# Performance work log

Hardware: AMD Instinct MI355X
Metric: run time of the kernel (lower is better)

## Reference

```python
import jax, jax.numpy as jnp
import numpy as np

V, E, U, D, B, T = 32000, 256, 512, 512, 32, 64


def setup_inputs() -> dict:
    key = jax.random.key(0)
    ks = jax.random.split(key, 12)
    g = lambda k, shape: (jax.random.normal(k, shape, jnp.float32) * 0.05)
    return dict(
        x=jax.random.randint(ks[0], (B, T), 0, V),
        emb=g(ks[1], (V, E)),
        Wxf=g(ks[2], (E, 4 * U)), Whf=g(ks[3], (U, 4 * U)), bf=jnp.zeros((4 * U,), jnp.float32),
        Wxb=g(ks[4], (E, 4 * U)), Whb=g(ks[5], (U, 4 * U)), bb=jnp.zeros((4 * U,), jnp.float32),
        W1=g(ks[6], (2 * U + D, 10)), b1=jnp.zeros((10,), jnp.float32),
        W2=g(ks[7], (10, 1)), b2=jnp.zeros((1,), jnp.float32),
        Wxd=g(ks[8], (2 * U, 4 * D)), Whd=g(ks[9], (D, 4 * D)), bd=jnp.zeros((4 * D,), jnp.float32),
        Wo=g(ks[10], (D, V)), bo=jnp.zeros((V,), jnp.float32),
    )


def lstm_cell(x_t, h, c, Wx, Wh, b):
    # Keras gate order: i, f, g(cell), o
    z = x_t @ Wx + h @ Wh + b
    i, f, g, o = jnp.split(z, 4, axis=-1)
    c = jax.nn.sigmoid(f) * c + jax.nn.sigmoid(i) * jnp.tanh(g)
    h = jax.nn.sigmoid(o) * jnp.tanh(c)
    return h, c


def lstm_seq(xs, Wx, Wh, b):
    # xs: [T, B, F] -> hidden states [T, B, units]
    units = Wh.shape[0]
    h0 = jnp.zeros((xs.shape[1], units), xs.dtype)

    def step(carry, x_t):
        h, c = lstm_cell(x_t, carry[0], carry[1], Wx, Wh, b)
        return (h, c), h

    _, hs = jax.lax.scan(step, (h0, h0), xs)
    return hs


def reference(x, emb, Wxf, Whf, bf, Wxb, Whb, bb, W1, b1, W2, b2, Wxd, Whd, bd, Wo, bo):
    Bsz, Tlen = x.shape
    xe = emb[x]                              # [B, T, E]
    xs = jnp.swapaxes(xe, 0, 1)              # [T, B, E]
    hf = lstm_seq(xs, Wxf, Whf, bf)          # forward direction
    hb = lstm_seq(xs[::-1], Wxb, Whb, bb)[::-1]  # backward direction
    a = jnp.swapaxes(jnp.concatenate([hf, hb], axis=-1), 0, 1)  # [B, T, 2U]
    du = Whd.shape[0]

    def dec_step(carry, _):
        h, c = carry
        s_rep = jnp.broadcast_to(h[:, None, :], (Bsz, Tlen, du))
        cat = jnp.concatenate([a, s_rep], axis=-1)              # [B, T, 2U+D]
        e = jax.nn.relu(jnp.tanh(cat @ W1 + b1) @ W2 + b2)      # [B, T, 1]
        score = jax.nn.softmax(e, axis=1)
        ctx = jnp.sum(score * a, axis=1)                        # [B, 2U]
        h, c = lstm_cell(ctx, h, c, Wxd, Whd, bd)
        out = jax.nn.softmax(h @ Wo + bo, axis=-1)              # [B, V]
        return (h, c), out

    init = (jnp.zeros((Bsz, du), a.dtype), jnp.zeros((Bsz, du), a.dtype))
    _, outs = jax.lax.scan(dec_step, init, None, length=Tlen)
    return jnp.swapaxes(outs, 0, 1)  # [B, T, V]
```

## Files before the change

kernel.cpp:

```cpp
#include <hip/hip_runtime.h>
#include <hip/hip_bf16.h>
#include <cstdint>

typedef float f32x4 __attribute__((ext_vector_type(4)));
typedef __bf16 bf16x8 __attribute__((ext_vector_type(8)));

__device__ __forceinline__ uint32_t bf1(float x) {
  uint32_t u = __float_as_uint(x);
  return (u + 0x7fffu + ((u >> 16) & 1u)) >> 16;
}
__device__ __forceinline__ uint32_t bpack(float lo, float hi) {
  return bf1(lo) | (bf1(hi) << 16);
}
__device__ __forceinline__ float blo(uint32_t u) { return __uint_as_float(u << 16); }
__device__ __forceinline__ float bhi(uint32_t u) { return __uint_as_float(u & 0xffff0000u); }
__device__ __forceinline__ float sigm(float x) {
  return __fdividef(1.f, 1.f + exp2f(x * -1.4426950408889634f));
}
__device__ __forceinline__ float tanhf_fast(float x) {
  float e2 = exp2f(x * 2.8853900817779268f);
  return 1.f - __fdividef(2.f, e2 + 1.f);
}

__device__ __forceinline__ float dot2bf(uint32_t a, uint32_t b, float acc) {
  asm("v_dot2_f32_bf16 %0, %1, %2, %0" : "+v"(acc) : "v"(a), "v"(b));
  return acc;
}

#define GLOAD_LDS16(g, l)                                                     \
  __builtin_amdgcn_global_load_lds(                                           \
      (const __attribute__((address_space(1))) void*)(g),                     \
      (__attribute__((address_space(3))) void*)(l), 16, 0, 0)

__global__ __launch_bounds__(256) void k0_enc(
    const float* __restrict__ Whf, const float* __restrict__ Whb,
    uint32_t* __restrict__ Wp)
{
  int p = blockIdx.x * 256 + threadIdx.x;
  int e = p & 3, c = (p >> 2) & 7, k4p = (p >> 5) & 63;
  int blk = (p >> 11) & 255, dir = p >> 19;
  int k2 = 4 * k4p + e;
  const float* W = dir ? Whb : Whf;
  int col = (c >> 1) * 512 + blk * 2 + (c & 1);
  float v0 = W[(size_t)(2 * k2) * 2048 + col];
  float v1 = W[(size_t)(2 * k2 + 1) * 2048 + col];
  Wp[p] = bpack(v0, v1);
}

__global__ __launch_bounds__(256) void k0_dec(
    const float* __restrict__ Whd, uint32_t* __restrict__ Wp)
{
  int p = blockIdx.x * 256 + threadIdx.x;
  int e = p & 3, cc = (p >> 2) & 31, q4 = (p >> 7) & 63, ug = p >> 13;
  int k2 = 4 * q4 + e;
  int col = (cc >> 3) * 512 + ug * 8 + (cc & 7);
  int k = 2 * k2;
  float v0 = Whd[(size_t)k * 2048 + col];
  float v1 = Whd[(size_t)(k + 1) * 2048 + col];
  Wp[p] = bpack(v0, v1);
}

__global__ __launch_bounds__(256) void k0_w1(
    const float* __restrict__ W1, uint32_t* __restrict__ W1pbAll)
{
  int p = blockIdx.x * 256 + threadIdx.x;
  int q = p / 12, j = p % 12;
  float v0 = (j < 10) ? W1[(size_t)(2 * q) * 10 + j] : 0.f;
  float v1 = (j < 10) ? W1[(size_t)(2 * q + 1) * 10 + j] : 0.f;
  W1pbAll[p] = bpack(v0, v1);
}

__global__ __launch_bounds__(256) void k1_embed_gemm(
    const int* __restrict__ x, const float* __restrict__ emb,
    const float* __restrict__ Wxf, const float* __restrict__ Wxb,
    const float* __restrict__ bfv, const float* __restrict__ bbv,
    float* __restrict__ Xf, float* __restrict__ Xb)
{
  __shared__ float As[32 * 260];
  __shared__ float Bs[32 * 128];
  __shared__ int xid[32];
  const int t = threadIdx.x;
  const int ty = blockIdx.y;
  const int c0 = blockIdx.x * 128;
  if (t < 32) xid[t] = x[t * 64 + ty];
  __syncthreads();
  for (int i = 0; i < 8; ++i) {
    int f4 = t + 256 * i;
    int r = f4 >> 6, k4 = (f4 & 63) << 2;
    float4 v = *(const float4*)(emb + (size_t)xid[r] * 256 + k4);
    *(float4*)(&As[r * 260 + k4]) = v;
  }
  const int isB = (c0 >= 2048);
  const float* Wsrc = isB ? Wxb : Wxf;
  const float* bias = isB ? bbv : bfv;
  const int cbase = c0 & 2047;
  float acc[4][4] = {};
  const int rq = t >> 5;
  const int cq = t & 31;
  for (int kc = 0; kc < 8; ++kc) {
    int k0 = kc * 32;
    __syncthreads();
    for (int i = 0; i < 4; ++i) {
      int f4 = t + 256 * i;
      int k = f4 >> 5, c4 = (f4 & 31) << 2;
      *(float4*)(&Bs[k * 128 + c4]) =
          *(const float4*)(Wsrc + (size_t)(k0 + k) * 2048 + cbase + c4);
    }
    __syncthreads();
#pragma unroll
    for (int kk = 0; kk < 32; ++kk) {
      float a0 = As[(4 * rq + 0) * 260 + k0 + kk];
      float a1 = As[(4 * rq + 1) * 260 + k0 + kk];
      float a2 = As[(4 * rq + 2) * 260 + k0 + kk];
      float a3 = As[(4 * rq + 3) * 260 + k0 + kk];
      float4 b = *(const float4*)(&Bs[kk * 128 + 4 * cq]);
      acc[0][0] += a0 * b.x; acc[0][1] += a0 * b.y; acc[0][2] += a0 * b.z; acc[0][3] += a0 * b.w;
      acc[1][0] += a1 * b.x; acc[1][1] += a1 * b.y; acc[1][2] += a1 * b.z; acc[1][3] += a1 * b.w;
      acc[2][0] += a2 * b.x; acc[2][1] += a2 * b.y; acc[2][2] += a2 * b.z; acc[2][3] += a2 * b.w;
      acc[3][0] += a3 * b.x; acc[3][1] += a3 * b.y; acc[3][2] += a3 * b.z; acc[3][3] += a3 * b.w;
    }
  }
  float* Xout = isB ? Xb : Xf;
  for (int i = 0; i < 4; ++i) {
    int c = cbase + 4 * cq + i;
    float bi = bias[c];
    for (int j = 0; j < 4; ++j) {
      int b_ = 4 * rq + j;
      Xout[((size_t)ty * 2048 + c) * 32 + b_] = acc[j][i] + bi;
    }
  }
}

__global__ __launch_bounds__(256) void k2_enc_step(
    const float* __restrict__ Xf, const float* __restrict__ Xb,
    const uint32_t* __restrict__ Wencp,
    const uint32_t* __restrict__ hfi, uint32_t* __restrict__ hfo,
    const uint32_t* __restrict__ hbi, uint32_t* __restrict__ hbo,
    float* __restrict__ cf, float* __restrict__ cb,
    ushort* __restrict__ aB, int step)
{
  __shared__ uint32_t hTp[256 * 32];
  __shared__ uint32_t Wsp[2048];
  __shared__ float zx[8 * 33];
  __shared__ float zbuf[32 * 9];
  __shared__ float hl[2 * 32];
  const int t = threadIdx.x;
  const int dir = blockIdx.x >> 8;
  const int blk = blockIdx.x & 255;
  const int u0 = blk * 2;
  const float* XF = dir ? Xb : Xf;
  const uint32_t* hin = dir ? hbi : hfi;
  uint32_t* hout = dir ? hbo : hfo;
  float* cst = dir ? cb : cf;
  const int ta = dir ? (63 - step) : step;
  const uint32_t* wsrc = Wencp + ((size_t)dir * 256 + blk) * 2048;

  for (int i = 0; i < 8; ++i) {
    int b4 = (t >> 6) * 64 + 256 * i;
    GLOAD_LDS16(hin + (size_t)(t + 256 * i) * 4, hTp + (size_t)b4 * 4);
  }
  for (int i = 0; i < 2; ++i) {
    int b4 = (t >> 6) * 64 + 256 * i;
    GLOAD_LDS16(wsrc + (size_t)(t + 256 * i) * 4, Wsp + (size_t)b4 * 4);
  }
  {
    int c = t >> 5, r = t & 31;
    int col = (c >> 1) * 512 + u0 + (c & 1);
    zx[c * 33 + r] = XF[((size_t)ta * 2048 + col) * 32 + r];
  }
  __syncthreads();
  const int r = t & 31, cc = t >> 5;
  float acc = zx[cc * 33 + r];
  const uint4* hT4 = (const uint4*)hTp;
  const uint4* Ws4 = (const uint4*)Wsp;
#pragma unroll 8
  for (int k4p = 0; k4p < 64; ++k4p) {
    uint4 ua = hT4[k4p * 32 + r];
    uint4 w = Ws4[k4p * 8 + cc];
    acc = dot2bf(ua.x, w.x, acc);
    acc = dot2bf(ua.y, w.y, acc);
    acc = dot2bf(ua.z, w.z, acc);
    acc = dot2bf(ua.w, w.w, acc);
  }
  zbuf[r * 9 + cc] = acc;
  __syncthreads();
  if (t < 64) {
    int rr = t & 31, j = t >> 5;
    float zi = zbuf[rr * 9 + j];
    float zf = zbuf[rr * 9 + 2 + j];
    float zg = zbuf[rr * 9 + 4 + j];
    float zo = zbuf[rr * 9 + 6 + j];
    int u = u0 + j;
    float cold = cst[u * 32 + rr];
    float cn = sigm(zf) * cold + sigm(zi) * tanhf_fast(zg);
    float h = sigm(zo) * tanhf_fast(cn);
    cst[u * 32 + rr] = cn;
    aB[((size_t)rr * 64 + ta) * 1024 + dir * 512 + u] = (ushort)bf1(h);
    hl[j * 32 + rr] = h;
  }
  __syncthreads();
  if (t < 32) {
    hout[(blk >> 2) * 128 + t * 4 + (blk & 3)] = bpack(hl[t], hl[32 + t]);
  }
}

__global__ __launch_bounds__(256) void k5_aw1(
    const ushort* __restrict__ aB, const uint32_t* __restrict__ W1pbAll,
    const float* __restrict__ b1, float* __restrict__ aw1)
{
  __shared__ uint32_t ar[512];
  __shared__ float ps[16 * 17];
  const int t = threadIdx.x;
  const uint32_t* aBu = (const uint32_t*)aB;
  for (int m = blockIdx.x; m < 2048; m += gridDim.x) {
    __syncthreads();
    *(uint2*)(&ar[t * 2]) = *(const uint2*)(aBu + (size_t)m * 512 + t * 2);
    __syncthreads();
    int j = t & 15, part = t >> 4;
    int jj = j < 10 ? j : 0;
    float s = 0.f;
#pragma unroll 8
    for (int q = part * 32; q < part * 32 + 32; ++q)
      s = dot2bf(ar[q], W1pbAll[q * 12 + jj], s);
    ps[part * 17 + j] = s;
    __syncthreads();
    if (t < 16) {
      float sum = 0.f;
      if (t < 10) {
        for (int p = 0; p < 16; ++p) sum += ps[p * 17 + t];
        sum += b1[t];
      }
      aw1[m * 16 + t] = sum;
    }
  }
}

__global__ __launch_bounds__(256) void k_wxdT(
    const float* __restrict__ Wxd, ushort* __restrict__ WxdT)
{
  __shared__ float tile[64 * 65];
  const int t = threadIdx.x;
  const int n0 = blockIdx.x * 64, k0 = blockIdx.y * 64;
  for (int i = 0; i < 16; ++i) {
    int p = t + 256 * i;
    int kk = p >> 6, nn = p & 63;
    tile[kk * 65 + nn] = Wxd[(size_t)(k0 + kk) * 2048 + n0 + nn];
  }
  __syncthreads();
  for (int i = 0; i < 4; ++i) {
    int p = t + 256 * i;
    int nn = p >> 4, k4 = (p & 15) * 4;
    ushort4 o;
    o.x = (ushort)bf1(tile[(k4 + 0) * 65 + nn]);
    o.y = (ushort)bf1(tile[(k4 + 1) * 65 + nn]);
    o.z = (ushort)bf1(tile[(k4 + 2) * 65 + nn]);
    o.w = (ushort)bf1(tile[(k4 + 3) * 65 + nn]);
    *(ushort4*)(WxdT + (size_t)(n0 + nn) * 1024 + k0 + k4) = o;
  }
}

__global__ __launch_bounds__(256) void kA_aprime(
    const ushort* __restrict__ WxdT, const ushort* __restrict__ aB,
    uint32_t* __restrict__ ApTb)
{
  __shared__ ushort As[128 * 64];
  __shared__ ushort Bs[128 * 64];
  const int t = threadIdx.x;
  const int lane = t & 63, w = t >> 6;
  const int wr = w >> 1, wc = w & 1;
  const int m0 = blockIdx.y * 128, n0 = blockIdx.x * 128;
  const int lrow = lane >> 3, s = lane & 7;
  const int quad = lane >> 4, l15 = lane & 15;
  f32x4 acc[4][4] = {};
  for (int kc = 0; kc < 16; ++kc) {
    const int k0 = kc * 64;
    __syncthreads();
    for (int i = 0; i < 4; ++i) {
      int row = w * 32 + i * 8 + lrow;
      int k8 = s ^ (row & 7);
      GLOAD_LDS16(WxdT + (size_t)(m0 + row) * 1024 + k0 + k8 * 8,
                  As + (w * 32 + i * 8) * 64);
      GLOAD_LDS16(aB + (size_t)(n0 + row) * 1024 + k0 + k8 * 8,
                  Bs + (w * 32 + i * 8) * 64);
    }
    __syncthreads();
#pragma unroll
    for (int ks = 0; ks < 2; ++ks) {
      bf16x8 af[4], bfr[4];
      int kq = ks * 4 + quad;
#pragma unroll
      for (int mi = 0; mi < 4; ++mi) {
        int row = wr * 64 + mi * 16 + l15;
        int slot = kq ^ (row & 7);
        af[mi] = *(const bf16x8*)(As + row * 64 + slot * 8);
      }
#pragma unroll
      for (int ni = 0; ni < 4; ++ni) {
        int row = wc * 64 + ni * 16 + l15;
        int slot = kq ^ (row & 7);
        bfr[ni] = *(const bf16x8*)(Bs + row * 64 + slot * 8);
      }
#pragma unroll
      for (int mi = 0; mi < 4; ++mi)
#pragma unroll
        for (int ni = 0; ni < 4; ++ni)
          acc[mi][ni] = __builtin_amdgcn_mfma_f32_16x16x32_bf16(
              af[mi], bfr[ni], acc[mi][ni], 0, 0, 0);
    }
  }
#pragma unroll
  for (int mi = 0; mi < 4; ++mi) {
    int mbase = m0 + wr * 64 + mi * 16 + quad * 4;
#pragma unroll
    for (int reg = 0; reg < 4; ++reg) {
      int m = mbase + reg;
#pragma unroll
      for (int ni = 0; ni < 4; ++ni) {
        int n = n0 + wc * 64 + ni * 16 + l15;
        float v = acc[mi][ni][reg];
        float v2 = __shfl_xor(v, 1);
        if (!(l15 & 1))
          ApTb[(size_t)m * 1024 + (n >> 1)] = bpack(v, v2);
      }
    }
  }
}

__global__ __launch_bounds__(256) void k4_dec_step(
    const uint32_t* __restrict__ ApTb, const float* __restrict__ aw1,
    const uint32_t* __restrict__ W1pb, const float* __restrict__ W2,
    const float* __restrict__ b2, const uint32_t* __restrict__ hdp_in,
    const uint32_t* __restrict__ Wdp, const float* __restrict__ bd,
    uint32_t* __restrict__ hdp_out, float* __restrict__ cd,
    ushort* __restrict__ HsB, int step)
{
  __shared__ uint32_t W1s[256 * 12];
  __shared__ uint32_t hdT[4096];
  __shared__ uint32_t Wsp[8192];
  __shared__ float ph[32 * 8 * 12];
  __shared__ float hw1[8 * 12];
  __shared__ float esc[8 * 65];
  __shared__ uint32_t escp[8 * 33];
  __shared__ float pm[8 * 9];
  __shared__ float mrow[8], srow[8];
  __shared__ float w2s[12];
  __shared__ float zbuf[8 * 33];
  __shared__ float hl[64];
  const int t = threadIdx.x;
  const int ug = blockIdx.x >> 2;
  const int rg = blockIdx.x & 3;
  const int u0 = ug * 8, r0 = rg * 8;
  for (int i = 0; i < 3; ++i) {
    int b4 = (t >> 6) * 64 + 256 * i;
    GLOAD_LDS16(W1pb + (size_t)(t + 256 * i) * 4, W1s + (size_t)b4 * 4);
  }
  for (int i = 0; i < 4; ++i) {
    int idx4 = t + 256 * i;
    int q4 = idx4 >> 3, rl = idx4 & 7;
    int b4 = (t >> 6) * 64 + 256 * i;
    GLOAD_LDS16(hdp_in + (size_t)(q4 * 32 + r0 + rl) * 4, hdT + (size_t)b4 * 4);
  }
  {
    const uint32_t* wsrc = Wdp + (size_t)ug * 8192;
    for (int i = 0; i < 8; ++i) {
      int b4 = (t >> 6) * 64 + 256 * i;
      GLOAD_LDS16(wsrc + (size_t)(t + 256 * i) * 4, Wsp + (size_t)b4 * 4);
    }
  }
  if (t < 12) w2s[t] = (t < 10) ? W2[t] : 0.f;
  __syncthreads();
  {
    const int rl = t & 7, kp = t >> 3;
    const uint4* hd4 = (const uint4*)hdT;
    float acc[10] = {};
    for (int q4 = kp * 2; q4 < kp * 2 + 2; ++q4) {
      uint4 u4 = hd4[q4 * 8 + rl];
      const uint32_t* w0 = &W1s[(4 * q4) * 12];
      const uint32_t* w1 = &W1s[(4 * q4 + 1) * 12];
      const uint32_t* w2p = &W1s[(4 * q4 + 2) * 12];
      const uint32_t* w3 = &W1s[(4 * q4 + 3) * 12];
#pragma unroll
      for (int j = 0; j < 10; ++j) {
        acc[j] = dot2bf(u4.x, w0[j], acc[j]);
        acc[j] = dot2bf(u4.y, w1[j], acc[j]);
        acc[j] = dot2bf(u4.z, w2p[j], acc[j]);
        acc[j] = dot2bf(u4.w, w3[j], acc[j]);
      }
    }
#pragma unroll
    for (int j = 0; j < 10; ++j) ph[(kp * 8 + rl) * 12 + j] = acc[j];
  }
  __syncthreads();
  if (t < 96) {
    int rl = t / 12, j = t % 12;
    float s = 0.f;
#pragma unroll
    for (int p = 0; p < 32; ++p) s += ph[(p * 8 + rl) * 12 + j];
    hw1[rl * 12 + j] = s;
  }
  __syncthreads();
  const float b2v = b2[0];
  for (int p = 0; p < 2; ++p) {
    int idx = t + 256 * p;
    int rl = idx >> 6, tt = idx & 63;
    size_t m = (size_t)(r0 + rl) * 64 + tt;
    const float4* aw = (const float4*)(aw1 + m * 16);
    float4 q0 = aw[0], q1 = aw[1], q2 = aw[2];
    const float* hw = &hw1[rl * 12];
    float e = b2v;
    e += tanhf_fast(q0.x + hw[0]) * w2s[0];
    e += tanhf_fast(q0.y + hw[1]) * w2s[1];
    e += tanhf_fast(q0.z + hw[2]) * w2s[2];
    e += tanhf_fast(q0.w + hw[3]) * w2s[3];
    e += tanhf_fast(q1.x + hw[4]) * w2s[4];
    e += tanhf_fast(q1.y + hw[5]) * w2s[5];
    e += tanhf_fast(q1.z + hw[6]) * w2s[6];
    e += tanhf_fast(q1.w + hw[7]) * w2s[7];
    e += tanhf_fast(q2.x + hw[8]) * w2s[8];
    e += tanhf_fast(q2.y + hw[9]) * w2s[9];
    esc[rl * 65 + tt] = fmaxf(e, 0.f);
  }
  __syncthreads();
  if (t < 64) {
    int rl = t >> 3, part = t & 7;
    float m = -1e30f;
    for (int i = 0; i < 8; ++i) m = fmaxf(m, esc[rl * 65 + part * 8 + i]);
    pm[rl * 9 + part] = m;
  }
  __syncthreads();
  if (t < 8) {
    float m = pm[t * 9];
    for (int p = 1; p < 8; ++p) m = fmaxf(m, pm[t * 9 + p]);
    mrow[t] = m;
  }
  __syncthreads();
  if (t < 64) {
    int rl = t >> 3, part = t & 7;
    float m = mrow[rl];
    float s = 0.f;
    for (int i = 0; i < 8; ++i) s += __expf(esc[rl * 65 + part * 8 + i] - m);
    pm[rl * 9 + part] = s;
  }
  __syncthreads();
  if (t < 8) {
    float s = 0.f;
    for (int p = 0; p < 8; ++p) s += pm[t * 9 + p];
    srow[t] = __fdividef(1.f, s);
  }
  __syncthreads();
  {
    int rl = t >> 5, q = t & 31;
    float m = mrow[rl], s = srow[rl];
    float v0 = __expf(esc[rl * 65 + 2 * q] - m) * s;
    float v1 = __expf(esc[rl * 65 + 2 * q + 1] - m) * s;
    escp[rl * 33 + q] = bpack(v0, v1);
  }
  __syncthreads();
  const int ccB = t >> 3, rl = t & 7;
  const int colg = (ccB >> 3) * 512 + u0 + (ccB & 7);
  float acc = 0.f;
  {
    const uint4* hd4 = (const uint4*)hdT;
    const uint4* wd4 = (const uint4*)Wsp;
#pragma unroll 8
    for (int q4 = 0; q4 < 64; ++q4) {
      uint4 ua = hd4[q4 * 8 + rl];
      uint4 ub = wd4[q4 * 32 + ccB];
      acc = dot2bf(ua.x, ub.x, acc);
      acc = dot2bf(ua.y, ub.y, acc);
      acc = dot2bf(ua.z, ub.z, acc);
      acc = dot2bf(ua.w, ub.w, acc);
    }
  }
  {
    const uint32_t* ap = ApTb + (size_t)colg * 1024 + (r0 + rl) * 32;
    const uint32_t* ep = &escp[rl * 33];
#pragma unroll
    for (int i8 = 0; i8 < 8; ++i8) {
      uint4 v = *(const uint4*)(ap + i8 * 4);
      acc = dot2bf(v.x, ep[4 * i8 + 0], acc);
      acc = dot2bf(v.y, ep[4 * i8 + 1], acc);
      acc = dot2bf(v.z, ep[4 * i8 + 2], acc);
      acc = dot2bf(v.w, ep[4 * i8 + 3], acc);
    }
  }
  zbuf[rl * 33 + ccB] = acc + bd[colg];
  __syncthreads();
  if (t < 64) {
    int j = t >> 3, rr = t & 7;
    int u = u0 + j, rgl = r0 + rr;
    float zi = zbuf[rr * 33 + j];
    float zf = zbuf[rr * 33 + 8 + j];
    float zg = zbuf[rr * 33 + 16 + j];
    float zo = zbuf[rr * 33 + 24 + j];
    float cold = cd[u * 32 + rgl];
    float cn = sigm(zf) * cold + sigm(zi) * tanhf_fast(zg);
    float h = sigm(zo) * tanhf_fast(cn);
    cd[u * 32 + rgl] = cn;
    HsB[(size_t)(step * 32 + rgl) * 512 + u] = (ushort)bf1(h);
    hl[j * 8 + rr] = h;
  }
  __syncthreads();
  if (t < 32) {
    int p = t >> 3, rr = t & 7;
    hdp_out[ug * 128 + (r0 + rr) * 4 + p] =
        bpack(hl[(2 * p) * 8 + rr], hl[(2 * p + 1) * 8 + rr]);
  }
}

__global__ __launch_bounds__(256) void k_woT(
    const float* __restrict__ Wo, ushort* __restrict__ WoT)
{
  __shared__ float tile[64 * 65];
  const int t = threadIdx.x;
  const int n0 = blockIdx.x * 64, k0 = blockIdx.y * 64;
  for (int i = 0; i < 16; ++i) {
    int p = t + 256 * i;
    int kk = p >> 6, nn = p & 63;
    tile[kk * 65 + nn] = Wo[(size_t)(k0 + kk) * 32000 + n0 + nn];
  }
  __syncthreads();
  for (int i = 0; i < 4; ++i) {
    int p = t + 256 * i;
    int nn = p >> 4, k4 = (p & 15) * 4;
    ushort4 o;
    o.x = (ushort)bf1(tile[(k4 + 0) * 65 + nn]);
    o.y = (ushort)bf1(tile[(k4 + 1) * 65 + nn]);
    o.z = (ushort)bf1(tile[(k4 + 2) * 65 + nn]);
    o.w = (ushort)bf1(tile[(k4 + 3) * 65 + nn]);
    *(ushort4*)(WoT + (size_t)(n0 + nn) * 512 + k0 + k4) = o;
  }
}

__global__ __launch_bounds__(256) void k6_logits_mfma(
    const ushort* __restrict__ HsB, const ushort* __restrict__ WoT,
    const float* __restrict__ bo, float* __restrict__ out,
    float2* __restrict__ pstats)
{
  __shared__ ushort As[128 * 64];
  __shared__ ushort Bs[128 * 64];
  const int t = threadIdx.x;
  const int lane = t & 63, w = t >> 6;
  const int wr = w >> 1, wc = w & 1;
  const int m0 = blockIdx.y * 128, n0 = blockIdx.x * 128;
  const int lrow = lane >> 3, s = lane & 7;
  const int quad = lane >> 4, l15 = lane & 15;
  f32x4 acc[4][4] = {};
  for (int kc = 0; kc < 8; ++kc) {
    const int k0 = kc * 64;
    __syncthreads();
    for (int i = 0; i < 4; ++i) {
      int row = w * 32 + i * 8 + lrow;
      int k8 = s ^ (row & 7);
      GLOAD_LDS16(HsB + (size_t)(m0 + row) * 512 + k0 + k8 * 8,
                  As + (w * 32 + i * 8) * 64);
      GLOAD_LDS16(WoT + (size_t)(n0 + row) * 512 + k0 + k8 * 8,
                  Bs + (w * 32 + i * 8) * 64);
    }
    __syncthreads();
#pragma unroll
    for (int ks = 0; ks < 2; ++ks) {
      bf16x8 af[4], bfr[4];
      int kq = ks * 4 + quad;
#pragma unroll
      for (int mi = 0; mi < 4; ++mi) {
        int row = wr * 64 + mi * 16 + l15;
        int slot = kq ^ (row & 7);
        af[mi] = *(const bf16x8*)(As + row * 64 + slot * 8);
      }
#pragma unroll
      for (int ni = 0; ni < 4; ++ni) {
        int row = wc * 64 + ni * 16 + l15;
        int slot = kq ^ (row & 7);
        bfr[ni] = *(const bf16x8*)(Bs + row * 64 + slot * 8);
      }
#pragma unroll
      for (int mi = 0; mi < 4; ++mi)
#pragma unroll
        for (int ni = 0; ni < 4; ++ni)
          acc[mi][ni] = __builtin_amdgcn_mfma_f32_16x16x32_bf16(
              af[mi], bfr[ni], acc[mi][ni], 0, 0, 0);
    }
  }
  __syncthreads();
  float* pmx = (float*)As;
  float* psm = (float*)Bs;
#pragma unroll
  for (int mi = 0; mi < 4; ++mi) {
    int mbase = m0 + wr * 64 + mi * 16 + quad * 4;
#pragma unroll
    for (int reg = 0; reg < 4; ++reg) {
      int m = mbase + reg;
      int rowl = (m - m0);
      size_t rowbase = ((size_t)(m & 31) * 64 + (m >> 5)) * 32000;
      float vs[4];
      float mx = -1e30f;
#pragma unroll
      for (int ni = 0; ni < 4; ++ni) {
        int n = n0 + wc * 64 + ni * 16 + l15;
        float v = acc[mi][ni][reg] + bo[n];
        out[rowbase + n] = v;
        vs[ni] = v;
        mx = fmaxf(mx, v);
      }
      float sl = __expf(vs[0] - mx) + __expf(vs[1] - mx) +
                 __expf(vs[2] - mx) + __expf(vs[3] - mx);
      pmx[rowl * 32 + wc * 16 + l15] = mx;
      psm[rowl * 32 + wc * 16 + l15] = sl;
    }
  }
  __syncthreads();
  if (t < 128) {
    float m = pmx[t * 32], sacc = psm[t * 32];
    for (int i = 1; i < 32; ++i) {
      float m2 = pmx[t * 32 + i], s2 = psm[t * 32 + i];
      float mn = fmaxf(m, m2);
      sacc = sacc * __expf(m - mn) + s2 * __expf(m2 - mn);
      m = mn;
    }
    int mg = m0 + t;
    int outrow = (mg & 31) * 64 + (mg >> 5);
    pstats[(size_t)outrow * 256 + blockIdx.x] = make_float2(m, sacc);
  }
}

__global__ __launch_bounds__(256) void k7_softmax(
    float* __restrict__ out, const float2* __restrict__ pstats)
{
  __shared__ float mred[256], sred[256];
  const int t = threadIdx.x;
  const int row = blockIdx.x;
  float m = -1e30f, s = 0.f;
  if (t < 250) {
    float2 p = pstats[(size_t)row * 256 + t];
    m = p.x;
    s = p.y;
  }
  mred[t] = m;
  sred[t] = s;
  __syncthreads();
  for (int st = 128; st > 0; st >>= 1) {
    if (t < st) {
      float m1 = mred[t], m2 = mred[t + st];
      float mn = fmaxf(m1, m2);
      sred[t] = sred[t] * __expf(m1 - mn) + sred[t + st] * __expf(m2 - mn);
      mred[t] = mn;
    }
    __syncthreads();
  }
  m = mred[0];
  const float inv = 1.f / sred[0];
  float* p = out + (size_t)row * 32000;
  for (int i = t; i < 8000; i += 256) {
    float4 v = *(const float4*)(p + i * 4);
    v.x = __expf(v.x - m) * inv;
    v.y = __expf(v.y - m) * inv;
    v.z = __expf(v.z - m) * inv;
    v.w = __expf(v.w - m) * inv;
    *(float4*)(p + i * 4) = v;
  }
}

extern "C" void kernel_launch(void* const* d_in, const int* in_sizes, int n_in,
                              void* d_out, int out_size, void* d_ws, size_t ws_size,
                              hipStream_t stream)
{
  const int* x = (const int*)d_in[0];
  const float* emb = (const float*)d_in[1];
  const float* Wxf = (const float*)d_in[2];
  const float* Whf = (const float*)d_in[3];
  const float* bfv = (const float*)d_in[4];
  const float* Wxb = (const float*)d_in[5];
  const float* Whb = (const float*)d_in[6];
  const float* bbv = (const float*)d_in[7];
  const float* W1 = (const float*)d_in[8];
  const float* b1 = (const float*)d_in[9];
  const float* W2 = (const float*)d_in[10];
  const float* b2 = (const float*)d_in[11];
  const float* Wxd = (const float*)d_in[12];
  const float* Whd = (const float*)d_in[13];
  const float* bd = (const float*)d_in[14];
  const float* Wo = (const float*)d_in[15];
  const float* bo = (const float*)d_in[16];

  float* ws = (float*)d_ws;
  float* c_f = ws + 0;
  float* c_b = ws + 16384;
  float* c_d = ws + 32768;
  uint32_t* hfp0 = (uint32_t*)(ws + 49152);
  uint32_t* hfp1 = hfp0 + 8192;
  uint32_t* hbp0 = (uint32_t*)(ws + 65536);
  uint32_t* hbp1 = hbp0 + 8192;
  uint32_t* hdp0 = (uint32_t*)(ws + 81920);
  uint32_t* hdp1 = hdp0 + 8192;
  uint32_t* W1pbAll = (uint32_t*)(ws + 98304);
  uint32_t* Wencp = (uint32_t*)(ws + 114688);
  uint32_t* Wdp = (uint32_t*)(ws + 1163264);
  ushort* aB = (ushort*)(ws + 1687552);
  float* aw1 = ws + 2742272;
  float* Xf = ws + 2775040;
  float* Xb = Xf + 4194304;
  ushort* HsB = (ushort*)(ws + 13260800);
  uint32_t* ApTb = (uint32_t*)Xf;
  ushort* WxdT = (ushort*)Xb;
  ushort* WoT = (ushort*)Xf;
  float2* pstats = (float2*)Wencp;

  hipMemsetAsync(ws, 0, 98304 * sizeof(float), stream);

  k0_enc<<<4096, 256, 0, stream>>>(Whf, Whb, Wencp);
  k0_dec<<<2048, 256, 0, stream>>>(Whd, Wdp);
  k0_w1<<<36, 256, 0, stream>>>(W1, W1pbAll);

  k1_embed_gemm<<<dim3(32, 64), 256, 0, stream>>>(x, emb, Wxf, Wxb, bfv, bbv, Xf, Xb);

  for (int s = 0; s < 64; ++s) {
    const uint32_t* hfi = (s & 1) ? hfp1 : hfp0;
    uint32_t* hfo = (s & 1) ? hfp0 : hfp1;
    const uint32_t* hbi = (s & 1) ? hbp1 : hbp0;
    uint32_t* hbo = (s & 1) ? hbp0 : hbp1;
    k2_enc_step<<<512, 256, 0, stream>>>(Xf, Xb, Wencp, hfi, hfo, hbi, hbo,
                                         c_f, c_b, aB, s);
  }

  k5_aw1<<<256, 256, 0, stream>>>(aB, W1pbAll, b1, aw1);
  k_wxdT<<<dim3(32, 16), 256, 0, stream>>>(Wxd, WxdT);
  kA_aprime<<<dim3(16, 16), 256, 0, stream>>>(WxdT, aB, ApTb);

  for (int s = 0; s < 64; ++s) {
    const uint32_t* hdi = (s & 1) ? hdp1 : hdp0;
    uint32_t* hdo = (s & 1) ? hdp0 : hdp1;
    k4_dec_step<<<256, 256, 0, stream>>>(ApTb, aw1, W1pbAll + 6144, W2, b2,
                                         hdi, Wdp, bd, hdo, c_d, HsB, s);
  }

  k_woT<<<dim3(500, 8), 256, 0, stream>>>(Wo, WoT);
  k6_logits_mfma<<<dim3(250, 16), 256, 0, stream>>>(HsB, WoT, bo,
                                                    (float*)d_out, pstats);
  k7_softmax<<<2048, 256, 0, stream>>>((float*)d_out, pstats);
}
```

Measured before the change: 1.635 ms.

## Merge weight-pack kernels, widen encoder step blocks, split logits/softmax into halves

```diff
diff --git a/kernel.cpp b/kernel.cpp
--- a/kernel.cpp
+++ b/kernel.cpp
@@ -32,42 +32,38 @@
       (const __attribute__((address_space(1))) void*)(g),                     \
       (__attribute__((address_space(3))) void*)(l), 16, 0, 0)
 
-__global__ __launch_bounds__(256) void k0_enc(
+__global__ __launch_bounds__(256) void k0_pack(
     const float* __restrict__ Whf, const float* __restrict__ Whb,
-    uint32_t* __restrict__ Wp)
-{
-  int p = blockIdx.x * 256 + threadIdx.x;
-  int e = p & 3, c = (p >> 2) & 7, k4p = (p >> 5) & 63;
-  int blk = (p >> 11) & 255, dir = p >> 19;
-  int k2 = 4 * k4p + e;
-  const float* W = dir ? Whb : Whf;
-  int col = (c >> 1) * 512 + blk * 2 + (c & 1);
-  float v0 = W[(size_t)(2 * k2) * 2048 + col];
-  float v1 = W[(size_t)(2 * k2 + 1) * 2048 + col];
-  Wp[p] = bpack(v0, v1);
-}
-
-__global__ __launch_bounds__(256) void k0_dec(
-    const float* __restrict__ Whd, uint32_t* __restrict__ Wp)
-{
-  int p = blockIdx.x * 256 + threadIdx.x;
-  int e = p & 3, cc = (p >> 2) & 31, q4 = (p >> 7) & 63, ug = p >> 13;
-  int k2 = 4 * q4 + e;
-  int col = (cc >> 3) * 512 + ug * 8 + (cc & 7);
-  int k = 2 * k2;
-  float v0 = Whd[(size_t)k * 2048 + col];
-  float v1 = Whd[(size_t)(k + 1) * 2048 + col];
-  Wp[p] = bpack(v0, v1);
-}
-
-__global__ __launch_bounds__(256) void k0_w1(
-    const float* __restrict__ W1, uint32_t* __restrict__ W1pbAll)
-{
-  int p = blockIdx.x * 256 + threadIdx.x;
-  int q = p / 12, j = p % 12;
-  float v0 = (j < 10) ? W1[(size_t)(2 * q) * 10 + j] : 0.f;
-  float v1 = (j < 10) ? W1[(size_t)(2 * q + 1) * 10 + j] : 0.f;
-  W1pbAll[p] = bpack(v0, v1);
+    uint32_t* __restrict__ Wencp, const float* __restrict__ Whd,
+    uint32_t* __restrict__ Wdp, const float* __restrict__ W1,
+    uint32_t* __restrict__ W1pbAll)
+{
+  int bid = blockIdx.x;
+  if (bid < 4096) {
+    int p = bid * 256 + threadIdx.x;
+    int e = p & 3, c = (p >> 2) & 15, k4p = (p >> 6) & 63;
+    int blk = (p >> 12) & 127, dir = p >> 19;
+    int k2 = 4 * k4p + e;
+    const float* W = dir ? Whb : Whf;
+    int col = (c >> 2) * 512 + blk * 4 + (c & 3);
+    Wencp[p] = bpack(W[(size_t)(2 * k2) * 2048 + col],
+                     W[(size_t)(2 * k2 + 1) * 2048 + col]);
+  } else if (bid < 6144) {
+    int p = (bid - 4096) * 256 + threadIdx.x;
+    int e = p & 3, cc = (p >> 2) & 31, q4 = (p >> 7) & 63, ug = p >> 13;
+    int k2 = 4 * q4 + e;
+    int col = (cc >> 3) * 512 + ug * 8 + (cc & 7);
+    int k = 2 * k2;
+    Wdp[p] = bpack(Whd[(size_t)k * 2048 + col], Whd[(size_t)(k + 1) * 2048 + col]);
+  } else {
+    int p = (bid - 6144) * 256 + threadIdx.x;
+    if (p < 9216) {
+      int q = p / 12, j = p % 12;
+      float v0 = (j < 10) ? W1[(size_t)(2 * q) * 10 + j] : 0.f;
+      float v1 = (j < 10) ? W1[(size_t)(2 * q + 1) * 10 + j] : 0.f;
+      W1pbAll[p] = bpack(v0, v1);
+    }
+  }
 }
 
 __global__ __launch_bounds__(256) void k1_embed_gemm(
@@ -139,57 +135,65 @@
     float* __restrict__ cf, float* __restrict__ cb,
     ushort* __restrict__ aB, int step)
 {
-  __shared__ uint32_t hTp[256 * 32];
-  __shared__ uint32_t Wsp[2048];
-  __shared__ float zx[8 * 33];
-  __shared__ float zbuf[32 * 9];
-  __shared__ float hl[2 * 32];
-  const int t = threadIdx.x;
-  const int dir = blockIdx.x >> 8;
-  const int blk = blockIdx.x & 255;
-  const int u0 = blk * 2;
+  __shared__ uint32_t hTp[8192];
+  __shared__ uint32_t Wsp[4096];
+  __shared__ float zx[16 * 33];
+  __shared__ float zbuf[32 * 17];
+  __shared__ float hl[4 * 32];
+  const int t = threadIdx.x;
+  const int dir = blockIdx.x >> 7;
+  const int blk = blockIdx.x & 127;
+  const int u0 = blk * 4;
   const float* XF = dir ? Xb : Xf;
   const uint32_t* hin = dir ? hbi : hfi;
   uint32_t* hout = dir ? hbo : hfo;
   float* cst = dir ? cb : cf;
   const int ta = dir ? (63 - step) : step;
-  const uint32_t* wsrc = Wencp + ((size_t)dir * 256 + blk) * 2048;
+  const uint32_t* wsrc = Wencp + ((size_t)dir * 128 + blk) * 4096;
 
   for (int i = 0; i < 8; ++i) {
     int b4 = (t >> 6) * 64 + 256 * i;
     GLOAD_LDS16(hin + (size_t)(t + 256 * i) * 4, hTp + (size_t)b4 * 4);
   }
-  for (int i = 0; i < 2; ++i) {
+  for (int i = 0; i < 4; ++i) {
     int b4 = (t >> 6) * 64 + 256 * i;
     GLOAD_LDS16(wsrc + (size_t)(t + 256 * i) * 4, Wsp + (size_t)b4 * 4);
   }
-  {
-    int c = t >> 5, r = t & 31;
-    int col = (c >> 1) * 512 + u0 + (c & 1);
+  for (int i = 0; i < 2; ++i) {
+    int p = t + 256 * i;
+    int c = p >> 5, r = p & 31;
+    int col = (c >> 2) * 512 + u0 + (c & 3);
     zx[c * 33 + r] = XF[((size_t)ta * 2048 + col) * 32 + r];
   }
   __syncthreads();
-  const int r = t & 31, cc = t >> 5;
-  float acc = zx[cc * 33 + r];
+  const int r = t & 31, slot = t >> 5;
+  float acc0 = zx[slot * 33 + r];
+  float acc1 = zx[(slot + 8) * 33 + r];
   const uint4* hT4 = (const uint4*)hTp;
   const uint4* Ws4 = (const uint4*)Wsp;
 #pragma unroll 8
   for (int k4p = 0; k4p < 64; ++k4p) {
     uint4 ua = hT4[k4p * 32 + r];
-    uint4 w = Ws4[k4p * 8 + cc];
-    acc = dot2bf(ua.x, w.x, acc);
-    acc = dot2bf(ua.y, w.y, acc);
-    acc = dot2bf(ua.z, w.z, acc);
-    acc = dot2bf(ua.w, w.w, acc);
-  }
-  zbuf[r * 9 + cc] = acc;
-  __syncthreads();
-  if (t < 64) {
+    uint4 w0 = Ws4[k4p * 16 + slot];
+    uint4 w1 = Ws4[k4p * 16 + slot + 8];
+    acc0 = dot2bf(ua.x, w0.x, acc0);
+    acc0 = dot2bf(ua.y, w0.y, acc0);
+    acc0 = dot2bf(ua.z, w0.z, acc0);
+    acc0 = dot2bf(ua.w, w0.w, acc0);
+    acc1 = dot2bf(ua.x, w1.x, acc1);
+    acc1 = dot2bf(ua.y, w1.y, acc1);
+    acc1 = dot2bf(ua.z, w1.z, acc1);
+    acc1 = dot2bf(ua.w, w1.w, acc1);
+  }
+  zbuf[r * 17 + slot] = acc0;
+  zbuf[r * 17 + slot + 8] = acc1;
+  __syncthreads();
+  if (t < 128) {
     int rr = t & 31, j = t >> 5;
-    float zi = zbuf[rr * 9 + j];
-    float zf = zbuf[rr * 9 + 2 + j];
-    float zg = zbuf[rr * 9 + 4 + j];
-    float zo = zbuf[rr * 9 + 6 + j];
+    float zi = zbuf[rr * 17 + j];
+    float zf = zbuf[rr * 17 + 4 + j];
+    float zg = zbuf[rr * 17 + 8 + j];
+    float zo = zbuf[rr * 17 + 12 + j];
     int u = u0 + j;
     float cold = cst[u * 32 + rr];
     float cn = sigm(zf) * cold + sigm(zi) * tanhf_fast(zg);
@@ -199,8 +203,11 @@
     hl[j * 32 + rr] = h;
   }
   __syncthreads();
-  if (t < 32) {
-    hout[(blk >> 2) * 128 + t * 4 + (blk & 3)] = bpack(hl[t], hl[32 + t]);
+  if (t < 64) {
+    int j = t >> 5, rr = t & 31;
+    int pair = blk * 2 + j;
+    hout[(pair >> 2) * 128 + rr * 4 + (pair & 3)] =
+        bpack(hl[(2 * j) * 32 + rr], hl[(2 * j + 1) * 32 + rr]);
   }
 }
 
@@ -356,10 +363,12 @@
   }
   for (int i = 0; i < 4; ++i) {
     int idx4 = t + 256 * i;
-    int q4 = idx4 >> 3, rl = idx4 & 7;
+    int q4 = idx4 >> 3, rl0 = idx4 & 7;
     int b4 = (t >> 6) * 64 + 256 * i;
-    GLOAD_LDS16(hdp_in + (size_t)(q4 * 32 + r0 + rl) * 4, hdT + (size_t)b4 * 4);
-  }
+    GLOAD_LDS16(hdp_in + (size_t)(q4 * 32 + r0 + rl0) * 4, hdT + (size_t)b4 * 4);
+  }
+  if (t < 12) w2s[t] = (t < 10) ? W2[t] : 0.f;
+  __syncthreads();
   {
     const uint32_t* wsrc = Wdp + (size_t)ug * 8192;
     for (int i = 0; i < 8; ++i) {
@@ -367,8 +376,6 @@
       GLOAD_LDS16(wsrc + (size_t)(t + 256 * i) * 4, Wsp + (size_t)b4 * 4);
     }
   }
-  if (t < 12) w2s[t] = (t < 10) ? W2[t] : 0.f;
-  __syncthreads();
   {
     const int rl = t & 7, kp = t >> 3;
     const uint4* hd4 = (const uint4*)hdT;
@@ -535,14 +542,14 @@
 __global__ __launch_bounds__(256) void k6_logits_mfma(
     const ushort* __restrict__ HsB, const ushort* __restrict__ WoT,
     const float* __restrict__ bo, float* __restrict__ out,
-    float2* __restrict__ pstats)
+    float2* __restrict__ pstats, int moff)
 {
   __shared__ ushort As[128 * 64];
   __shared__ ushort Bs[128 * 64];
   const int t = threadIdx.x;
   const int lane = t & 63, w = t >> 6;
   const int wr = w >> 1, wc = w & 1;
-  const int m0 = blockIdx.y * 128, n0 = blockIdx.x * 128;
+  const int m0 = (blockIdx.y + moff) * 128, n0 = blockIdx.x * 128;
   const int lrow = lane >> 3, s = lane & 7;
   const int quad = lane >> 4, l15 = lane & 15;
   f32x4 acc[4][4] = {};
@@ -625,11 +632,12 @@
 }
 
 __global__ __launch_bounds__(256) void k7_softmax(
-    float* __restrict__ out, const float2* __restrict__ pstats)
+    float* __restrict__ out, const float2* __restrict__ pstats, int half)
 {
   __shared__ float mred[256], sred[256];
   const int t = threadIdx.x;
-  const int row = blockIdx.x;
+  const int mg = half * 1024 + blockIdx.x;
+  const int row = (mg & 31) * 64 + (mg >> 5);
   float m = -1e30f, s = 0.f;
   if (t < 250) {
     float2 p = pstats[(size_t)row * 256 + t];
@@ -708,9 +716,7 @@
 
   hipMemsetAsync(ws, 0, 98304 * sizeof(float), stream);
 
-  k0_enc<<<4096, 256, 0, stream>>>(Whf, Whb, Wencp);
-  k0_dec<<<2048, 256, 0, stream>>>(Whd, Wdp);
-  k0_w1<<<36, 256, 0, stream>>>(W1, W1pbAll);
+  k0_pack<<<6180, 256, 0, stream>>>(Whf, Whb, Wencp, Whd, Wdp, W1, W1pbAll);
 
   k1_embed_gemm<<<dim3(32, 64), 256, 0, stream>>>(x, emb, Wxf, Wxb, bfv, bbv, Xf, Xb);
 
@@ -719,7 +725,7 @@
     uint32_t* hfo = (s & 1) ? hfp0 : hfp1;
     const uint32_t* hbi = (s & 1) ? hbp1 : hbp0;
     uint32_t* hbo = (s & 1) ? hbp0 : hbp1;
-    k2_enc_step<<<512, 256, 0, stream>>>(Xf, Xb, Wencp, hfi, hfo, hbi, hbo,
+    k2_enc_step<<<256, 256, 0, stream>>>(Xf, Xb, Wencp, hfi, hfo, hbi, hbo,
                                          c_f, c_b, aB, s);
   }
 
@@ -735,7 +741,10 @@
   }
 
   k_woT<<<dim3(500, 8), 256, 0, stream>>>(Wo, WoT);
-  k6_logits_mfma<<<dim3(250, 16), 256, 0, stream>>>(HsB, WoT, bo,
-                                                    (float*)d_out, pstats);
-  k7_softmax<<<2048, 256, 0, stream>>>((float*)d_out, pstats);
-}
+  k6_logits_mfma<<<dim3(250, 8), 256, 0, stream>>>(HsB, WoT, bo,
+                                                   (float*)d_out, pstats, 0);
+  k7_softmax<<<1024, 256, 0, stream>>>((float*)d_out, pstats, 0);
+  k6_logits_mfma<<<dim3(250, 8), 256, 0, stream>>>(HsB, WoT, bo,
+                                                   (float*)d_out, pstats, 8);
+  k7_softmax<<<1024, 256, 0, stream>>>((float*)d_out, pstats, 1);
+}
```

Measured after the change: 1.657 ms. About the same (+1.3%).

## Merge weight-pack kernels, split logits/softmax into halves, reorder dec-step loads

Applied to the files above, without the earlier changes.

```diff
diff --git a/kernel.cpp b/kernel.cpp
--- a/kernel.cpp
+++ b/kernel.cpp
@@ -32,42 +32,38 @@
       (const __attribute__((address_space(1))) void*)(g),                     \
       (__attribute__((address_space(3))) void*)(l), 16, 0, 0)
 
-__global__ __launch_bounds__(256) void k0_enc(
+__global__ __launch_bounds__(256) void k0_pack(
     const float* __restrict__ Whf, const float* __restrict__ Whb,
-    uint32_t* __restrict__ Wp)
-{
-  int p = blockIdx.x * 256 + threadIdx.x;
-  int e = p & 3, c = (p >> 2) & 7, k4p = (p >> 5) & 63;
-  int blk = (p >> 11) & 255, dir = p >> 19;
-  int k2 = 4 * k4p + e;
-  const float* W = dir ? Whb : Whf;
-  int col = (c >> 1) * 512 + blk * 2 + (c & 1);
-  float v0 = W[(size_t)(2 * k2) * 2048 + col];
-  float v1 = W[(size_t)(2 * k2 + 1) * 2048 + col];
-  Wp[p] = bpack(v0, v1);
-}
-
-__global__ __launch_bounds__(256) void k0_dec(
-    const float* __restrict__ Whd, uint32_t* __restrict__ Wp)
-{
-  int p = blockIdx.x * 256 + threadIdx.x;
-  int e = p & 3, cc = (p >> 2) & 31, q4 = (p >> 7) & 63, ug = p >> 13;
-  int k2 = 4 * q4 + e;
-  int col = (cc >> 3) * 512 + ug * 8 + (cc & 7);
-  int k = 2 * k2;
-  float v0 = Whd[(size_t)k * 2048 + col];
-  float v1 = Whd[(size_t)(k + 1) * 2048 + col];
-  Wp[p] = bpack(v0, v1);
-}
-
-__global__ __launch_bounds__(256) void k0_w1(
-    const float* __restrict__ W1, uint32_t* __restrict__ W1pbAll)
-{
-  int p = blockIdx.x * 256 + threadIdx.x;
-  int q = p / 12, j = p % 12;
-  float v0 = (j < 10) ? W1[(size_t)(2 * q) * 10 + j] : 0.f;
-  float v1 = (j < 10) ? W1[(size_t)(2 * q + 1) * 10 + j] : 0.f;
-  W1pbAll[p] = bpack(v0, v1);
+    uint32_t* __restrict__ Wencp, const float* __restrict__ Whd,
+    uint32_t* __restrict__ Wdp, const float* __restrict__ W1,
+    uint32_t* __restrict__ W1pbAll)
+{
+  int bid = blockIdx.x;
+  if (bid < 4096) {
+    int p = bid * 256 + threadIdx.x;
+    int e = p & 3, c = (p >> 2) & 7, k4p = (p >> 5) & 63;
+    int blk = (p >> 11) & 255, dir = p >> 19;
+    int k2 = 4 * k4p + e;
+    const float* W = dir ? Whb : Whf;
+    int col = (c >> 1) * 512 + blk * 2 + (c & 1);
+    Wencp[p] = bpack(W[(size_t)(2 * k2) * 2048 + col],
+                     W[(size_t)(2 * k2 + 1) * 2048 + col]);
+  } else if (bid < 6144) {
+    int p = (bid - 4096) * 256 + threadIdx.x;
+    int e = p & 3, cc = (p >> 2) & 31, q4 = (p >> 7) & 63, ug = p >> 13;
+    int k2 = 4 * q4 + e;
+    int col = (cc >> 3) * 512 + ug * 8 + (cc & 7);
+    int k = 2 * k2;
+    Wdp[p] = bpack(Whd[(size_t)k * 2048 + col], Whd[(size_t)(k + 1) * 2048 + col]);
+  } else {
+    int p = (bid - 6144) * 256 + threadIdx.x;
+    if (p < 9216) {
+      int q = p / 12, j = p % 12;
+      float v0 = (j < 10) ? W1[(size_t)(2 * q) * 10 + j] : 0.f;
+      float v1 = (j < 10) ? W1[(size_t)(2 * q + 1) * 10 + j] : 0.f;
+      W1pbAll[p] = bpack(v0, v1);
+    }
+  }
 }
 
 __global__ __launch_bounds__(256) void k1_embed_gemm(
@@ -356,10 +352,12 @@
   }
   for (int i = 0; i < 4; ++i) {
     int idx4 = t + 256 * i;
-    int q4 = idx4 >> 3, rl = idx4 & 7;
+    int q4 = idx4 >> 3, rl0 = idx4 & 7;
     int b4 = (t >> 6) * 64 + 256 * i;
-    GLOAD_LDS16(hdp_in + (size_t)(q4 * 32 + r0 + rl) * 4, hdT + (size_t)b4 * 4);
-  }
+    GLOAD_LDS16(hdp_in + (size_t)(q4 * 32 + r0 + rl0) * 4, hdT + (size_t)b4 * 4);
+  }
+  if (t < 12) w2s[t] = (t < 10) ? W2[t] : 0.f;
+  __syncthreads();
   {
     const uint32_t* wsrc = Wdp + (size_t)ug * 8192;
     for (int i = 0; i < 8; ++i) {
@@ -367,8 +365,6 @@
       GLOAD_LDS16(wsrc + (size_t)(t + 256 * i) * 4, Wsp + (size_t)b4 * 4);
     }
   }
-  if (t < 12) w2s[t] = (t < 10) ? W2[t] : 0.f;
-  __syncthreads();
   {
     const int rl = t & 7, kp = t >> 3;
     const uint4* hd4 = (const uint4*)hdT;
@@ -535,14 +531,14 @@
 __global__ __launch_bounds__(256) void k6_logits_mfma(
     const ushort* __restrict__ HsB, const ushort* __restrict__ WoT,
     const float* __restrict__ bo, float* __restrict__ out,
-    float2* __restrict__ pstats)
+    float2* __restrict__ pstats, int moff)
 {
   __shared__ ushort As[128 * 64];
   __shared__ ushort Bs[128 * 64];
   const int t = threadIdx.x;
   const int lane = t & 63, w = t >> 6;
   const int wr = w >> 1, wc = w & 1;
-  const int m0 = blockIdx.y * 128, n0 = blockIdx.x * 128;
+  const int m0 = (blockIdx.y + moff) * 128, n0 = blockIdx.x * 128;
   const int lrow = lane >> 3, s = lane & 7;
   const int quad = lane >> 4, l15 = lane & 15;
   f32x4 acc[4][4] = {};
@@ -625,11 +621,12 @@
 }
 
 __global__ __launch_bounds__(256) void k7_softmax(
-    float* __restrict__ out, const float2* __restrict__ pstats)
+    float* __restrict__ out, const float2* __restrict__ pstats, int half)
 {
   __shared__ float mred[256], sred[256];
   const int t = threadIdx.x;
-  const int row = blockIdx.x;
+  const int mg = half * 1024 + blockIdx.x;
+  const int row = (mg & 31) * 64 + (mg >> 5);
   float m = -1e30f, s = 0.f;
   if (t < 250) {
     float2 p = pstats[(size_t)row * 256 + t];
@@ -708,9 +705,7 @@
 
   hipMemsetAsync(ws, 0, 98304 * sizeof(float), stream);
 
-  k0_enc<<<4096, 256, 0, stream>>>(Whf, Whb, Wencp);
-  k0_dec<<<2048, 256, 0, stream>>>(Whd, Wdp);
-  k0_w1<<<36, 256, 0, stream>>>(W1, W1pbAll);
+  k0_pack<<<6180, 256, 0, stream>>>(Whf, Whb, Wencp, Whd, Wdp, W1, W1pbAll);
 
   k1_embed_gemm<<<dim3(32, 64), 256, 0, stream>>>(x, emb, Wxf, Wxb, bfv, bbv, Xf, Xb);
 
@@ -735,7 +730,10 @@
   }
 
   k_woT<<<dim3(500, 8), 256, 0, stream>>>(Wo, WoT);
-  k6_logits_mfma<<<dim3(250, 16), 256, 0, stream>>>(HsB, WoT, bo,
-                                                    (float*)d_out, pstats);
-  k7_softmax<<<2048, 256, 0, stream>>>((float*)d_out, pstats);
-}
+  k6_logits_mfma<<<dim3(250, 8), 256, 0, stream>>>(HsB, WoT, bo,
+                                                   (float*)d_out, pstats, 0);
+  k7_softmax<<<1024, 256, 0, stream>>>((float*)d_out, pstats, 0);
+  k6_logits_mfma<<<dim3(250, 8), 256, 0, stream>>>(HsB, WoT, bo,
+                                                   (float*)d_out, pstats, 8);
+  k7_softmax<<<1024, 256, 0, stream>>>((float*)d_out, pstats, 1);
+}
```

After: 1.634 ms. No clear change (-0.0%).
